# Optimization experiments

Hardware: AMD Instinct MI355X
Metric: run time of the kernel (lower is better)

## Reference

```python
import jax, jax.numpy as jnp
import numpy as np

BLOCK = 128
FP8_MAX = 448.0


def _quantize_weight_blockwise(w):
    """Blockwise fp8 quantization of weight [O, I] -> (fp8-valued f32 weight, [O/B, I/B] scales)."""
    O, I = w.shape
    wb = w.reshape(O // BLOCK, BLOCK, I // BLOCK, BLOCK)
    amax = jnp.maximum(jnp.max(jnp.abs(wb), axis=(1, 3), keepdims=True), 1e-12)
    scale = amax / FP8_MAX  # [O/B,1,I/B,1]
    w_fp8 = (wb / scale).astype(jnp.float8_e4m3fn).astype(jnp.float32).reshape(O, I)
    return w_fp8, scale[:, 0, :, 0]


def setup_inputs() -> dict:
    key = jax.random.key(0)
    k1, k2 = jax.random.split(key)
    tokens, input_size, output_size = 8192, 4096, 4096
    x = jax.random.normal(k1, (tokens, input_size), dtype=jnp.float32)
    w_hp = jax.random.normal(k2, (output_size, input_size), dtype=jnp.float32) * 0.02
    weight, weight_scale_inv = _quantize_weight_blockwise(w_hp)
    return {"x": x, "weight": weight, "weight_scale_inv": weight_scale_inv}


def reference(x, weight, weight_scale_inv):
    # --- dynamic per-token fp8 quantization of activations ---
    amax = jnp.maximum(jnp.max(jnp.abs(x), axis=-1, keepdims=True), 1e-12)  # [T,1]
    x_scale = amax / FP8_MAX                                                # [T,1] f32
    x_fp8 = (x / x_scale).astype(jnp.float8_e4m3fn).astype(jnp.float32)     # fp8-valued f32
    # --- blockwise dequant of fp8 weight with weight_scale_inv ---
    O, I = weight.shape
    scale_full = jnp.repeat(jnp.repeat(weight_scale_inv, BLOCK, axis=0), BLOCK, axis=1)  # [O,I]
    w_deq = weight * scale_full
    # --- fp8 block-scaled GEMM (dequantized-equivalent math) ---
    y = jnp.einsum('tk,ok->to', x_fp8, w_deq) * x_scale  # [T, O]
    return y
```

## Files before the change

kernel.cpp:

```cpp
#include <hip/hip_runtime.h>
#include <stdint.h>

#define FP8_MAX 448.0f
#define TOKENS  8192
#define IDIM    4096
#define ODIM    4096

typedef float f32x4 __attribute__((ext_vector_type(4)));
typedef int   i32x4 __attribute__((ext_vector_type(4)));
typedef int   i32x8 __attribute__((ext_vector_type(8)));

__device__ __forceinline__ void async_copy16(const uint8_t* g, uint8_t* l) {
  __builtin_amdgcn_global_load_lds((const __attribute__((address_space(1))) void*)g,
                                   (__attribute__((address_space(3))) void*)l,
                                   16, 0, 0);
}

__global__ __launch_bounds__(256) void prep_kernel(
    const float* __restrict__ x, const float* __restrict__ w,
    uint8_t* __restrict__ xq, uint8_t* __restrict__ wq, float* __restrict__ xsc) {
  const int lane = threadIdx.x & 63;
  const int wid  = threadIdx.x >> 6;

  if (blockIdx.x < 2048) {
    const int row = blockIdx.x * 4 + wid;
    const f32x4* xr = (const f32x4*)(x + (size_t)row * IDIM);

    f32x4 v[16];
    float amax = 0.0f;
    #pragma unroll
    for (int k = 0; k < 16; k++) {
      v[k] = xr[lane + k * 64];
      amax = fmaxf(amax, fmaxf(fmaxf(fabsf(v[k].x), fabsf(v[k].y)),
                               fmaxf(fabsf(v[k].z), fabsf(v[k].w))));
    }
    #pragma unroll
    for (int off = 32; off > 0; off >>= 1)
      amax = fmaxf(amax, __shfl_xor(amax, off, 64));
    amax = fmaxf(amax, 1e-12f);
    const float scale = amax / FP8_MAX;
    if (lane == 0) xsc[row] = scale;

    uint32_t* out = (uint32_t*)(xq + (size_t)row * IDIM);
    #pragma unroll
    for (int k = 0; k < 16; k++) {
      float a = v[k].x / scale, b = v[k].y / scale;
      float c = v[k].z / scale, d = v[k].w / scale;
      int p = __builtin_amdgcn_cvt_pk_fp8_f32(a, b, 0, false);
      p = __builtin_amdgcn_cvt_pk_fp8_f32(c, d, p, true);
      out[lane + k * 64] = (uint32_t)p;
    }
  } else {
    const int row = (blockIdx.x - 2048) * 4 + wid;
    const f32x4* wp = (const f32x4*)(w + (size_t)row * IDIM);
    uint32_t* out = (uint32_t*)(wq + (size_t)row * IDIM);
    #pragma unroll
    for (int k = 0; k < 16; k++) {
      f32x4 t = wp[lane + k * 64];
      int p = __builtin_amdgcn_cvt_pk_fp8_f32(t.x, t.y, 0, false);
      p = __builtin_amdgcn_cvt_pk_fp8_f32(t.z, t.w, p, true);
      out[lane + k * 64] = (uint32_t)p;
    }
  }
}

__global__ __launch_bounds__(256) void gemm_fp8_kernel(
    const uint8_t* __restrict__ xq, const uint8_t* __restrict__ wq,
    const float* __restrict__ xsc, const float* __restrict__ wsi,
    float* __restrict__ y) {
  __shared__ __align__(16) uint8_t As0[128 * 128];
  __shared__ __align__(16) uint8_t Bs0[128 * 128];
  __shared__ __align__(16) uint8_t As1[128 * 128];
  __shared__ __align__(16) uint8_t Bs1[128 * 128];

  const int tid  = threadIdx.x;
  const int bo   = blockIdx.x & 31;
  const int bt   = blockIdx.x >> 5;
  const int t0   = bt << 7;
  const int o0   = bo << 7;
  const int lane = tid & 63;
  const int wave = tid >> 6;
  const int wr   = (wave >> 1) << 6;
  const int wc   = (wave & 1) << 6;
  const int ln   = lane & 15;
  const int quad = lane >> 4;

  const int rb  = tid >> 3;
  const int cs  = ((tid & 7) ^ (rb & 7)) << 4;
  const int lds = tid << 4;

  const int c0 = quad << 1;
  int aoff[4][2], boff[4][2];
  #pragma unroll
  for (int i = 0; i < 4; i++) {
    const int ra = wr + i * 16 + ln;
    const int sa = ra & 7;
    aoff[i][0] = ra * 128 + ((c0 ^ sa) << 4);
    aoff[i][1] = ra * 128 + (((c0 + 1) ^ sa) << 4);
    const int rb2 = wc + i * 16 + ln;
    const int sb = rb2 & 7;
    boff[i][0] = rb2 * 128 + ((c0 ^ sb) << 4);
    boff[i][1] = rb2 * 128 + (((c0 + 1) ^ sb) << 4);
  }

  f32x4 outer[4][4];
  #pragma unroll
  for (int i = 0; i < 4; i++)
    #pragma unroll
    for (int j = 0; j < 4; j++)
      outer[i][j] = (f32x4)(0.0f);

  const float* wsrow = wsi + bo * 32;
  const int ident = 0x7f7f7f7f;
  const f32x4 zero4 = (f32x4)(0.0f);

  auto stage = [&](uint8_t* Ad, uint8_t* Bd, int kb) {
    const int k0 = kb << 7;
    #pragma unroll
    for (int u = 0; u < 4; u++) {
      async_copy16(xq + ((size_t)(t0 + u * 32 + rb) << 12) + (k0 + cs),
                   Ad + u * 4096 + lds);
      async_copy16(wq + ((size_t)(o0 + u * 32 + rb) << 12) + (k0 + cs),
                   Bd + u * 4096 + lds);
    }
  };

  auto compute = [&](const uint8_t* Ab, const uint8_t* Bb, float s) {
    i32x8 a[4], b[4];
    #pragma unroll
    for (int i = 0; i < 4; i++) {
      i32x4 alo = *(const i32x4*)(Ab + aoff[i][0]);
      i32x4 ahi = *(const i32x4*)(Ab + aoff[i][1]);
      a[i] = __builtin_shufflevector(alo, ahi, 0, 1, 2, 3, 4, 5, 6, 7);
      i32x4 blo = *(const i32x4*)(Bb + boff[i][0]);
      i32x4 bhi = *(const i32x4*)(Bb + boff[i][1]);
      b[i] = __builtin_shufflevector(blo, bhi, 0, 1, 2, 3, 4, 5, 6, 7);
    }
    #pragma unroll
    for (int i = 0; i < 4; i++)
      #pragma unroll
      for (int j = 0; j < 4; j++) {
        f32x4 t = __builtin_amdgcn_mfma_scale_f32_16x16x128_f8f6f4(
            a[i], b[j], zero4, 0, 0, 0, ident, 0, ident);
        outer[i][j] += s * t;
      }
  };

  stage(As0, Bs0, 0);
  __syncthreads();

  for (int kb = 0; kb < 32; kb += 2) {
    if (kb + 1 < 32) stage(As1, Bs1, kb + 1);
    compute(As0, Bs0, wsrow[kb]);
    __syncthreads();

    if (kb + 2 < 32) stage(As0, Bs0, kb + 2);
    compute(As1, Bs1, wsrow[kb + 1]);
    __syncthreads();
  }

  #pragma unroll
  for (int i = 0; i < 4; i++) {
    #pragma unroll
    for (int r = 0; r < 4; r++) {
      const int t = t0 + wr + i * 16 + quad * 4 + r;
      const float sc = xsc[t];
      float* yp = y + ((size_t)t << 12) + o0 + wc + ln;
      #pragma unroll
      for (int j = 0; j < 4; j++)
        yp[j * 16] = outer[i][j][r] * sc;
    }
  }
}

extern "C" void kernel_launch(void* const* d_in, const int* in_sizes, int n_in,
                              void* d_out, int out_size, void* d_ws, size_t ws_size,
                              hipStream_t stream) {
  const float* x   = (const float*)d_in[0];
  const float* w   = (const float*)d_in[1];
  const float* wsi = (const float*)d_in[2];
  float* y = (float*)d_out;

  uint8_t* xq = (uint8_t*)d_ws;
  uint8_t* wq = xq + (size_t)TOKENS * IDIM;
  float*  xsc = (float*)(wq + (size_t)ODIM * IDIM);

  prep_kernel<<<3072, 256, 0, stream>>>(x, w, xq, wq, xsc);
  gemm_fp8_kernel<<<2048, 256, 0, stream>>>(xq, wq, xsc, wsi, y);
}
```

Baseline: 438.0 us.

## Add dedicated producer wave for async LDS staging in fp8 GEMM

The GEMM block grows from four to five waves. The extra wave issues every global-to-LDS async copy for both double-buffered A and B tiles, while the four compute waves only run MFMA work between barriers. The barrier counts on both sides match, so the ping-pong schedule is kept. The goal is to take load-address arithmetic and copy issue off the MFMA waves so they can overlap better. The cost is that one wave must now issue all 32 copies per stage, and the new launch bounds of 320 threads with 3 blocks may tighten the register budget.

```diff
diff --git a/kernel.cpp b/kernel.cpp
--- a/kernel.cpp
+++ b/kernel.cpp
@@ -64,7 +64,7 @@
   }
 }
 
-__global__ __launch_bounds__(256) void gemm_fp8_kernel(
+__global__ __launch_bounds__(320, 3) void gemm_fp8_kernel(
     const uint8_t* __restrict__ xq, const uint8_t* __restrict__ wq,
     const float* __restrict__ xsc, const float* __restrict__ wsi,
     float* __restrict__ y) {
@@ -80,14 +80,42 @@
   const int o0   = bo << 7;
   const int lane = tid & 63;
   const int wave = tid >> 6;
+
+  if (wave == 4) {
+    const int r8 = lane >> 3;
+    const int c8 = lane & 7;
+    auto stage_full = [&](uint8_t* Ad, uint8_t* Bd, int k0) {
+      #pragma unroll
+      for (int v = 0; v < 16; v++) {
+        const int row = v * 8 + r8;
+        const int chunk = (c8 ^ (row & 7)) << 4;
+        async_copy16(xq + ((size_t)(t0 + row) << 12) + k0 + chunk,
+                     Ad + v * 1024 + (lane << 4));
+      }
+      #pragma unroll
+      for (int v = 0; v < 16; v++) {
+        const int row = v * 8 + r8;
+        const int chunk = (c8 ^ (row & 7)) << 4;
+        async_copy16(wq + ((size_t)(o0 + row) << 12) + k0 + chunk,
+                     Bd + v * 1024 + (lane << 4));
+      }
+    };
+
+    stage_full(As0, Bs0, 0);
+    __syncthreads();
+    for (int kb = 0; kb < 32; kb += 2) {
+      stage_full(As1, Bs1, (kb + 1) << 7);
+      __syncthreads();
+      if (kb + 2 < 32) stage_full(As0, Bs0, (kb + 2) << 7);
+      __syncthreads();
+    }
+    return;
+  }
+
   const int wr   = (wave >> 1) << 6;
   const int wc   = (wave & 1) << 6;
   const int ln   = lane & 15;
   const int quad = lane >> 4;
-
-  const int rb  = tid >> 3;
-  const int cs  = ((tid & 7) ^ (rb & 7)) << 4;
-  const int lds = tid << 4;
 
   const int c0 = quad << 1;
   int aoff[4][2], boff[4][2];
@@ -114,17 +142,6 @@
   const int ident = 0x7f7f7f7f;
   const f32x4 zero4 = (f32x4)(0.0f);
 
-  auto stage = [&](uint8_t* Ad, uint8_t* Bd, int kb) {
-    const int k0 = kb << 7;
-    #pragma unroll
-    for (int u = 0; u < 4; u++) {
-      async_copy16(xq + ((size_t)(t0 + u * 32 + rb) << 12) + (k0 + cs),
-                   Ad + u * 4096 + lds);
-      async_copy16(wq + ((size_t)(o0 + u * 32 + rb) << 12) + (k0 + cs),
-                   Bd + u * 4096 + lds);
-    }
-  };
-
   auto compute = [&](const uint8_t* Ab, const uint8_t* Bb, float s) {
     i32x8 a[4], b[4];
     #pragma unroll
@@ -146,15 +163,10 @@
       }
   };
 
-  stage(As0, Bs0, 0);
   __syncthreads();
-
   for (int kb = 0; kb < 32; kb += 2) {
-    if (kb + 1 < 32) stage(As1, Bs1, kb + 1);
     compute(As0, Bs0, wsrow[kb]);
     __syncthreads();
-
-    if (kb + 2 < 32) stage(As0, Bs0, kb + 2);
     compute(As1, Bs1, wsrow[kb + 1]);
     __syncthreads();
   }
@@ -186,5 +198,5 @@
   float*  xsc = (float*)(wq + (size_t)ODIM * IDIM);
 
   prep_kernel<<<3072, 256, 0, stream>>>(x, w, xq, wq, xsc);
-  gemm_fp8_kernel<<<2048, 256, 0, stream>>>(xq, wq, xsc, wsi, y);
-}
+  gemm_fp8_kernel<<<2048, 320, 0, stream>>>(xq, wq, xsc, wsi, y);
+}
```

Result: slower. 515.1 us (+17.6%).
